# Kernel optimization log

Measured on AMD Instinct MI355X. Metric: run time of the kernel, lower is better.

Reference implementation:

```python
import jax, jax.numpy as jnp
import numpy as np

OBS_DIM, ACT_DIM, LATENT_DIM, BELIEF_DIM, T = 128, 32, 512, 1024, 32768


def setup_inputs() -> dict:
    key = jax.random.key(0)
    ks = jax.random.split(key, 8)
    s_ih = 1.0 / np.sqrt(BELIEF_DIM)
    s_enc = 1.0 / np.sqrt(OBS_DIM)
    return {
        "obs_seq": jax.random.normal(ks[0], (T, OBS_DIM), jnp.float32),
        "act_seq": jax.random.normal(ks[1], (T, ACT_DIM), jnp.float32),
        "enc_w": jax.random.uniform(ks[2], (LATENT_DIM, OBS_DIM), jnp.float32, -s_enc, s_enc),
        "enc_b": jax.random.uniform(ks[3], (LATENT_DIM,), jnp.float32, -s_enc, s_enc),
        "w_ih": jax.random.uniform(ks[4], (3 * BELIEF_DIM, LATENT_DIM + ACT_DIM), jnp.float32, -s_ih, s_ih),
        "w_hh": jax.random.uniform(ks[5], (3 * BELIEF_DIM, BELIEF_DIM), jnp.float32, -s_ih, s_ih),
        "b_ih": jax.random.uniform(ks[6], (3 * BELIEF_DIM,), jnp.float32, -s_ih, s_ih),
        "b_hh": jax.random.uniform(ks[7], (3 * BELIEF_DIM,), jnp.float32, -s_ih, s_ih),
    }


def reference(obs_seq, act_seq, enc_w, enc_b, w_ih, w_hh, b_ih, b_hh):
    H = w_hh.shape[1]
    # Encoder over all timesteps at once: (T, latent)
    z_seq = jnp.tanh(obs_seq @ enc_w.T + enc_b)
    # a_prev[t] = act_seq[t-1], zeros at t=0
    a_prev = jnp.concatenate(
        [jnp.zeros((1, act_seq.shape[1]), act_seq.dtype), act_seq[:-1]], axis=0)
    x_seq = jnp.concatenate([z_seq, a_prev], axis=-1)  # (T, latent+act)
    # Precompute input-side gate projections as one big GEMM: (T, 3H)
    gi_seq = x_seq @ w_ih.T + b_ih

    def step(h, gi_t):
        gh = w_hh @ h + b_hh  # (3H,)
        ir, iz, inn = jnp.split(gi_t, 3)
        hr, hz, hn = jnp.split(gh, 3)
        r = jax.nn.sigmoid(ir + hr)
        z = jax.nn.sigmoid(iz + hz)
        n = jnp.tanh(inn + r * hn)
        h_new = (1.0 - z) * n + z * h
        return h_new, h_new

    h0 = jnp.zeros((H,), x_seq.dtype)
    _, beliefs = jax.lax.scan(step, h0, gi_seq)
    return beliefs  # (T, belief_dim)
```

## Files before the change

### kernel.cpp

```cpp
#include <hip/hip_runtime.h>
#include <stdint.h>

#define T_STEPS 32768
#define HDIM    1024
#define LDIM    512
#define ADIM    32
#define NWG     128
#define NOUT    8
#define NREP    16

__global__ __launch_bounds__(256) void encoder_kernel(
    const float* __restrict__ obs,
    const float* __restrict__ w,
    const float* __restrict__ b,
    float* __restrict__ z)
{
    __shared__ float As[64][65];
    __shared__ float Bs[64][65];

    const int tile_n = blockIdx.x;
    const int tile_t = blockIdx.y;
    const int tid = threadIdx.x;
    const int ty = tid >> 4;
    const int tx = tid & 15;

    float acc[4][4] = {};

    for (int kt = 0; kt < 2; ++kt) {
        #pragma unroll
        for (int it = 0; it < 4; ++it) {
            int lin = it * 1024 + tid * 4;
            int r = lin >> 6, c = lin & 63;
            float4 va = *(const float4*)&obs[(size_t)(tile_t * 64 + r) * 128 + kt * 64 + c];
            As[r][c] = va.x; As[r][c+1] = va.y; As[r][c+2] = va.z; As[r][c+3] = va.w;
            float4 vb = *(const float4*)&w[(size_t)(tile_n * 64 + r) * 128 + kt * 64 + c];
            Bs[r][c] = vb.x; Bs[r][c+1] = vb.y; Bs[r][c+2] = vb.z; Bs[r][c+3] = vb.w;
        }
        __syncthreads();

        for (int k = 0; k < 64; ++k) {
            float av[4], bv[4];
            #pragma unroll
            for (int a = 0; a < 4; ++a) av[a] = As[ty * 4 + a][k];
            #pragma unroll
            for (int c = 0; c < 4; ++c) bv[c] = Bs[tx * 4 + c][k];
            #pragma unroll
            for (int a = 0; a < 4; ++a)
                #pragma unroll
                for (int c = 0; c < 4; ++c)
                    acc[a][c] = fmaf(av[a], bv[c], acc[a][c]);
        }
        __syncthreads();
    }

    #pragma unroll
    for (int a = 0; a < 4; ++a) {
        int row = tile_t * 64 + ty * 4 + a;
        #pragma unroll
        for (int c = 0; c < 4; ++c) {
            int col = tile_n * 64 + tx * 4 + c;
            z[(size_t)row * LDIM + col] = tanhf(acc[a][c] + b[col]);
        }
    }
}

__global__ __launch_bounds__(256, 1) void gru_kernel(
    float* __restrict__ out,
    const float* __restrict__ z_seq,
    const float* __restrict__ act,
    const float* __restrict__ w_ih,
    const float* __restrict__ w_hh,
    const float* __restrict__ b_ih,
    const float* __restrict__ b_hh,
    uint64_t* __restrict__ hbuf)
{
    __shared__ float h_lds[HDIM];
    __shared__ float z_lds[LDIM];
    __shared__ float a_lds[ADIM];
    __shared__ float h_pub[NOUT];

    const int tid  = threadIdx.x;
    const int wg   = blockIdx.x;
    const int grp  = tid >> 5;
    const int lane = tid & 31;
    const int i    = wg * NOUT + grp;

    float whr[32], whz[32], whn[32];
    {
        const float* pr = &w_hh[(size_t)i * HDIM + lane];
        const float* pz = &w_hh[(size_t)(HDIM + i) * HDIM + lane];
        const float* pn = &w_hh[(size_t)(2 * HDIM + i) * HDIM + lane];
        #pragma unroll
        for (int j = 0; j < 32; ++j) {
            whr[j] = pr[32 * j]; whz[j] = pz[32 * j]; whn[j] = pn[32 * j];
        }
    }
    float wir[17], wiz[17], win[17];
    {
        const float* pr = &w_ih[(size_t)i * 544 + lane];
        const float* pz = &w_ih[(size_t)(HDIM + i) * 544 + lane];
        const float* pn = &w_ih[(size_t)(2 * HDIM + i) * 544 + lane];
        #pragma unroll
        for (int j = 0; j < 17; ++j) {
            wir[j] = pr[32 * j]; wiz[j] = pz[32 * j]; win[j] = pn[32 * j];
        }
    }
    #pragma unroll
    for (int j = 0; j < 32; ++j) {
        asm volatile("" : "+v"(whr[j]), "+v"(whz[j]), "+v"(whn[j]));
    }
    #pragma unroll
    for (int j = 0; j < 17; ++j) {
        asm volatile("" : "+v"(wir[j]), "+v"(wiz[j]), "+v"(win[j]));
    }

    const float bir  = b_ih[i], biz = b_ih[HDIM + i], bin_ = b_ih[2 * HDIM + i];
    const float bhr  = b_hh[i], bhz = b_hh[HDIM + i], bhn  = b_hh[2 * HDIM + i];

    for (int q = tid; q < HDIM; q += 256) h_lds[q] = 0.0f;
    __syncthreads();

    for (int t = 0; t < T_STEPS; ++t) {
        if (tid < 128) {
            float4 v = *(const float4*)&z_seq[(size_t)t * LDIM + tid * 4];
            *(float4*)&z_lds[tid * 4] = v;
            if (tid < ADIM) {
                a_lds[tid] = (t == 0) ? 0.0f : act[(size_t)(t - 1) * ADIM + tid];
            }
        } else if (t > 0) {
            const int q = tid - 128;
            const uint64_t* bp = hbuf + ((size_t)((t - 1) & 1)) * 16384
                                      + q * 128 + (wg & (NREP - 1)) * 8;
            const uint32_t want = (uint32_t)t;
            uint64_t v[8];
            int done = 0;
            while (done != 0xFF) {
                #pragma unroll
                for (int k = 0; k < 8; ++k) {
                    if (!(done & (1 << k))) {
                        v[k] = __hip_atomic_load(bp + k, __ATOMIC_RELAXED,
                                                 __HIP_MEMORY_SCOPE_AGENT);
                    }
                }
                #pragma unroll
                for (int k = 0; k < 8; ++k) {
                    if (!(done & (1 << k)) && (uint32_t)(v[k] >> 32) == want)
                        done |= (1 << k);
                }
            }
            float4 h0, h1;
            h0.x = __uint_as_float((uint32_t)v[0]);
            h0.y = __uint_as_float((uint32_t)v[1]);
            h0.z = __uint_as_float((uint32_t)v[2]);
            h0.w = __uint_as_float((uint32_t)v[3]);
            h1.x = __uint_as_float((uint32_t)v[4]);
            h1.y = __uint_as_float((uint32_t)v[5]);
            h1.z = __uint_as_float((uint32_t)v[6]);
            h1.w = __uint_as_float((uint32_t)v[7]);
            *(float4*)&h_lds[q * 8]     = h0;
            *(float4*)&h_lds[q * 8 + 4] = h1;
        }
        __syncthreads();

        float sr = 0.f, sz = 0.f, sn = 0.f;
        #pragma unroll
        for (int j = 0; j < 32; ++j) {
            float hv = h_lds[lane + 32 * j];
            sr = fmaf(whr[j], hv, sr);
            sz = fmaf(whz[j], hv, sz);
            sn = fmaf(whn[j], hv, sn);
        }
        float gr = 0.f, gz = 0.f, gn = 0.f;
        #pragma unroll
        for (int j = 0; j < 16; ++j) {
            float xv = z_lds[lane + 32 * j];
            gr = fmaf(wir[j], xv, gr);
            gz = fmaf(wiz[j], xv, gz);
            gn = fmaf(win[j], xv, gn);
        }
        {
            float xa = a_lds[lane];
            gr = fmaf(wir[16], xa, gr);
            gz = fmaf(wiz[16], xa, gz);
            gn = fmaf(win[16], xa, gn);
        }

        float vr = sr + gr, vz = sz + gz;
        #pragma unroll
        for (int m = 16; m >= 1; m >>= 1) {
            vr += __shfl_xor(vr, m);
            vz += __shfl_xor(vz, m);
            sn += __shfl_xor(sn, m);
            gn += __shfl_xor(gn, m);
        }

        if (lane == 0) {
            float r  = 1.0f / (1.0f + expf(-(vr + bir + bhr)));
            float zg = 1.0f / (1.0f + expf(-(vz + biz + bhz)));
            float n  = tanhf(gn + bin_ + r * (sn + bhn));
            float hold = h_lds[i];
            h_pub[grp] = (1.0f - zg) * n + zg * hold;
        }
        __syncthreads();

        if (tid < 128) {
            uint64_t pk = ((uint64_t)(uint32_t)(t + 1) << 32) |
                          (uint64_t)__float_as_uint(h_pub[tid & 7]);
            __hip_atomic_store(&hbuf[((size_t)(t & 1)) * 16384 + wg * 128 + tid],
                               pk, __ATOMIC_RELAXED, __HIP_MEMORY_SCOPE_AGENT);
            if (tid < NOUT) {
                out[(size_t)t * HDIM + wg * NOUT + tid] = h_pub[tid];
            }
        }
    }
}

extern "C" void kernel_launch(void* const* d_in, const int* in_sizes, int n_in,
                              void* d_out, int out_size, void* d_ws, size_t ws_size,
                              hipStream_t stream) {
    const float* obs   = (const float*)d_in[0];
    const float* act   = (const float*)d_in[1];
    const float* enc_w = (const float*)d_in[2];
    const float* enc_b = (const float*)d_in[3];
    const float* w_ih  = (const float*)d_in[4];
    const float* w_hh  = (const float*)d_in[5];
    const float* b_ih  = (const float*)d_in[6];
    const float* b_hh  = (const float*)d_in[7];
    float* out = (float*)d_out;

    uint64_t* hbuf  = (uint64_t*)d_ws;
    float*    z_seq = (float*)((char*)d_ws + 262144);

    hipMemsetAsync(hbuf, 0, 262144, stream);

    encoder_kernel<<<dim3(8, 512), 256, 0, stream>>>(obs, enc_w, enc_b, z_seq);

    void* args[] = {(void*)&out, (void*)&z_seq, (void*)&act, (void*)&w_ih,
                    (void*)&w_hh, (void*)&b_ih, (void*)&b_hh, (void*)&hbuf};
    hipLaunchCooperativeKernel((void*)gru_kernel, dim3(NWG), dim3(256),
                               args, 0, stream);
}
```

Baseline: 105.0 ms.

## Remove second barrier per step, drop hbuf replication, prefetch inputs, use fast math

Each step's new hidden value is now published by lane 0 straight to a single, non-replicated flag-tagged buffer. This removes the shared staging array and the second __syncthreads per timestep. z/act inputs for the next step are prefetched into double-buffered LDS during the matvec, and h uses ping-pong LDS buffers. Sigmoid and tanh switch to __expf plus a hardware reciprocal, which reduces precision. With no replicas, all 128 workgroups poll the same cache lines, which may add contention.

Measured after the change: 118.3 ms. +12.6%, slower.

```diff
diff --git a/kernel.cpp b/kernel.cpp
--- a/kernel.cpp
+++ b/kernel.cpp
@@ -7,7 +7,15 @@
 #define ADIM    32
 #define NWG     128
 #define NOUT    8
-#define NREP    16
+
+__device__ __forceinline__ float fast_sigmoid(float x) {
+    float e = __expf(-x);
+    return __builtin_amdgcn_rcpf(1.0f + e);
+}
+__device__ __forceinline__ float fast_tanh(float x) {
+    float e = __expf(2.0f * x);
+    return 1.0f - 2.0f * __builtin_amdgcn_rcpf(1.0f + e);
+}
 
 __global__ __launch_bounds__(256) void encoder_kernel(
     const float* __restrict__ obs,
@@ -74,10 +82,9 @@
     const float* __restrict__ b_hh,
     uint64_t* __restrict__ hbuf)
 {
-    __shared__ float h_lds[HDIM];
-    __shared__ float z_lds[LDIM];
-    __shared__ float a_lds[ADIM];
-    __shared__ float h_pub[NOUT];
+    __shared__ float h_lds[2][HDIM];
+    __shared__ float z_lds[2][LDIM];
+    __shared__ float a_lds[2][ADIM];
 
     const int tid  = threadIdx.x;
     const int wg   = blockIdx.x;
@@ -114,23 +121,27 @@
         asm volatile("" : "+v"(wir[j]), "+v"(wiz[j]), "+v"(win[j]));
     }
 
-    const float bir  = b_ih[i], biz = b_ih[HDIM + i], bin_ = b_ih[2 * HDIM + i];
-    const float bhr  = b_hh[i], bhz = b_hh[HDIM + i], bhn  = b_hh[2 * HDIM + i];
-
-    for (int q = tid; q < HDIM; q += 256) h_lds[q] = 0.0f;
+    const float bias_r = b_ih[i] + b_hh[i];
+    const float bias_z = b_ih[HDIM + i] + b_hh[HDIM + i];
+    const float bin_   = b_ih[2 * HDIM + i];
+    const float bhn    = b_hh[2 * HDIM + i];
+
+    for (int q = tid; q < HDIM; q += 256) h_lds[1][q] = 0.0f;
+    if (tid < 128) {
+        float4 v = *(const float4*)&z_seq[tid * 4];
+        *(float4*)&z_lds[0][tid * 4] = v;
+        if (tid < 8) *(float4*)&a_lds[0][tid * 4] = make_float4(0.f, 0.f, 0.f, 0.f);
+    }
+    float hold = 0.0f;
     __syncthreads();
 
     for (int t = 0; t < T_STEPS; ++t) {
-        if (tid < 128) {
-            float4 v = *(const float4*)&z_seq[(size_t)t * LDIM + tid * 4];
-            *(float4*)&z_lds[tid * 4] = v;
-            if (tid < ADIM) {
-                a_lds[tid] = (t == 0) ? 0.0f : act[(size_t)(t - 1) * ADIM + tid];
-            }
-        } else if (t > 0) {
+        const int cur = t & 1;
+        const int pb  = (t + 1) & 1;
+
+        if (tid >= 128 && t > 0) {
             const int q = tid - 128;
-            const uint64_t* bp = hbuf + ((size_t)((t - 1) & 1)) * 16384
-                                      + q * 128 + (wg & (NREP - 1)) * 8;
+            const uint64_t* bp = hbuf + (size_t)pb * HDIM + q * 8;
             const uint32_t want = (uint32_t)t;
             uint64_t v[8];
             int done = 0;
@@ -157,15 +168,24 @@
             h1.y = __uint_as_float((uint32_t)v[5]);
             h1.z = __uint_as_float((uint32_t)v[6]);
             h1.w = __uint_as_float((uint32_t)v[7]);
-            *(float4*)&h_lds[q * 8]     = h0;
-            *(float4*)&h_lds[q * 8 + 4] = h1;
+            *(float4*)&h_lds[pb][q * 8]     = h0;
+            *(float4*)&h_lds[pb][q * 8 + 4] = h1;
         }
         __syncthreads();
 
+        float4 zpre, apre;
+        if (tid < 128) {
+            int tn = (t + 1 < T_STEPS) ? (t + 1) : t;
+            zpre = *(const float4*)&z_seq[(size_t)tn * LDIM + tid * 4];
+            if (tid < 8) {
+                apre = *(const float4*)&act[(size_t)t * ADIM + tid * 4];
+            }
+        }
+
         float sr = 0.f, sz = 0.f, sn = 0.f;
         #pragma unroll
         for (int j = 0; j < 32; ++j) {
-            float hv = h_lds[lane + 32 * j];
+            float hv = h_lds[pb][lane + 32 * j];
             sr = fmaf(whr[j], hv, sr);
             sz = fmaf(whz[j], hv, sz);
             sn = fmaf(whn[j], hv, sn);
@@ -173,13 +193,13 @@
         float gr = 0.f, gz = 0.f, gn = 0.f;
         #pragma unroll
         for (int j = 0; j < 16; ++j) {
-            float xv = z_lds[lane + 32 * j];
+            float xv = z_lds[cur][lane + 32 * j];
             gr = fmaf(wir[j], xv, gr);
             gz = fmaf(wiz[j], xv, gz);
             gn = fmaf(win[j], xv, gn);
         }
         {
-            float xa = a_lds[lane];
+            float xa = a_lds[cur][lane];
             gr = fmaf(wir[16], xa, gr);
             gz = fmaf(wiz[16], xa, gz);
             gn = fmaf(win[16], xa, gn);
@@ -195,22 +215,21 @@
         }
 
         if (lane == 0) {
-            float r  = 1.0f / (1.0f + expf(-(vr + bir + bhr)));
-            float zg = 1.0f / (1.0f + expf(-(vz + biz + bhz)));
-            float n  = tanhf(gn + bin_ + r * (sn + bhn));
-            float hold = h_lds[i];
-            h_pub[grp] = (1.0f - zg) * n + zg * hold;
-        }
-        __syncthreads();
+            float r    = fast_sigmoid(vr + bias_r);
+            float zg   = fast_sigmoid(vz + bias_z);
+            float n    = fast_tanh(gn + bin_ + r * (sn + bhn));
+            float hnew = (1.0f - zg) * n + zg * hold;
+            hold = hnew;
+            uint64_t pk = ((uint64_t)(uint32_t)(t + 1) << 32) |
+                          (uint64_t)__float_as_uint(hnew);
+            __hip_atomic_store(&hbuf[(size_t)cur * HDIM + i], pk,
+                               __ATOMIC_RELAXED, __HIP_MEMORY_SCOPE_AGENT);
+            out[(size_t)t * HDIM + i] = hnew;
+        }
 
         if (tid < 128) {
-            uint64_t pk = ((uint64_t)(uint32_t)(t + 1) << 32) |
-                          (uint64_t)__float_as_uint(h_pub[tid & 7]);
-            __hip_atomic_store(&hbuf[((size_t)(t & 1)) * 16384 + wg * 128 + tid],
-                               pk, __ATOMIC_RELAXED, __HIP_MEMORY_SCOPE_AGENT);
-            if (tid < NOUT) {
-                out[(size_t)t * HDIM + wg * NOUT + tid] = h_pub[tid];
-            }
+            *(float4*)&z_lds[cur ^ 1][tid * 4] = zpre;
+            if (tid < 8) *(float4*)&a_lds[cur ^ 1][tid * 4] = apre;
         }
     }
 }
@@ -229,9 +248,9 @@
     float* out = (float*)d_out;
 
     uint64_t* hbuf  = (uint64_t*)d_ws;
-    float*    z_seq = (float*)((char*)d_ws + 262144);
-
-    hipMemsetAsync(hbuf, 0, 262144, stream);
+    float*    z_seq = (float*)((char*)d_ws + 65536);
+
+    hipMemsetAsync(hbuf, 0, 2 * HDIM * sizeof(uint64_t), stream);
 
     encoder_kernel<<<dim3(8, 512), 256, 0, stream>>>(obs, enc_w, enc_b, z_seq);
 
```
